# Optimization experiments

Hardware: AMD Instinct MI355X
Metric: run time of the kernel (lower is better)

The kernel has to match this reference:

```python
import jax, jax.numpy as jnp
import numpy as np

B, L, H = 2, 2048, 1024
E = H * 2          # mamba_dim = model_dim * expansion_factor
K = 4              # conv kernel size
N = 16             # SSM state dim
DT_RANK = H // 8   # 128, mamba default ceil(d_model/16) scaled on d_inner


def setup_inputs() -> dict:
    key = jax.random.key(0)
    ks = jax.random.split(key, 12)
    s = lambda fan_in: 1.0 / np.sqrt(fan_in)
    return {
        "x": jax.random.normal(ks[0], (B, L, H), jnp.float32),
        "W_in": jax.random.normal(ks[1], (H, 2 * E), jnp.float32) * s(H),
        "b_in": jnp.zeros((2 * E,), jnp.float32),
        "conv_w": jax.random.normal(ks[2], (E, 1, K), jnp.float32) * s(K),  # depthwise OIH
        "conv_b": jnp.zeros((E,), jnp.float32),
        "x_proj_w": jax.random.normal(ks[3], (E, DT_RANK + 2 * N), jnp.float32) * s(E),
        "dt_proj_w": jax.random.normal(ks[4], (DT_RANK, E), jnp.float32) * s(DT_RANK),
        "dt_bias": jax.random.uniform(ks[5], (E,), jnp.float32, -4.0, -2.0),  # softplus(.) small
        "A_log": jnp.log(jnp.broadcast_to(jnp.arange(1, N + 1, dtype=jnp.float32), (E, N))),
        "D_param": jnp.ones((E,), jnp.float32),
        "W_out": jax.random.normal(ks[6], (E, H), jnp.float32) * s(E),
        "b_out": jnp.zeros((H,), jnp.float32),
    }


def _selective_scan(u, delta, A, Bm, Cm, Dp):
    # u, delta: (B,L,E); A: (E,N); Bm, Cm: (B,L,N); Dp: (E,)
    def step(h, inp):
        d_t, u_t, b_t, c_t = inp          # (B,E), (B,E), (B,N), (B,N)
        dA = jnp.exp(d_t[..., None] * A)  # (B,E,N)
        h = dA * h + (d_t * u_t)[..., None] * b_t[:, None, :]
        y = jnp.einsum("ben,bn->be", h, c_t)
        return h, y

    h0 = jnp.zeros((u.shape[0], A.shape[0], A.shape[1]), u.dtype)
    xs = (delta.transpose(1, 0, 2), u.transpose(1, 0, 2),
          Bm.transpose(1, 0, 2), Cm.transpose(1, 0, 2))
    _, ys = jax.lax.scan(step, h0, xs)    # ys: (L,B,E)
    return ys.transpose(1, 0, 2) + u * Dp


def reference(x, W_in, b_in, conv_w, conv_b, x_proj_w, dt_proj_w, dt_bias,
              A_log, D_param, W_out, b_out):
    silu = jax.nn.silu
    z = x @ W_in + b_in                    # (B,L,2E)
    xc, xr = z[..., :E], z[..., E:]
    xr = silu(xr)
    # causal depthwise conv1d: left-pad K-1 (== torch pad=K-1 then truncate to L)
    xt = xc.transpose(0, 2, 1)             # (B,E,L)
    xt = jax.lax.conv_general_dilated(
        xt, conv_w, window_strides=(1,), padding=[(K - 1, 0)],
        feature_group_count=E, dimension_numbers=("NCH", "OIH", "NCH"))
    xc = silu((xt + conv_b[None, :, None]).transpose(0, 2, 1))  # (B,L,E)
    # S6 selective SSM
    proj = xc @ x_proj_w                   # (B,L,dt_rank+2N)
    dt = proj[..., :DT_RANK]
    Bm = proj[..., DT_RANK:DT_RANK + N]
    Cm = proj[..., DT_RANK + N:]
    delta = jax.nn.softplus(dt @ dt_proj_w + dt_bias)  # (B,L,E)
    A = -jnp.exp(A_log)                    # (E,N)
    y = _selective_scan(xc, delta, A, Bm, Cm, D_param)
    y = y * xr                             # gate
    return y @ W_out + b_out
```

## Files before the change

### kernel.cpp

```cpp
#include <hip/hip_runtime.h>
#include <cstdint>

#define SL 2048
#define SE 2048
#define SB 2
#define SN 16
#define SC 64
#define ST 32

enum { EP_SPLIT_SILU = 1, EP_BIAS = 3, EP_PARTIAL = 4 };

typedef __attribute__((ext_vector_type(8))) short bf16x8;
typedef __attribute__((ext_vector_type(4))) float f32x4;

__device__ __forceinline__ float silu_f(float x) { return x / (1.f + __expf(-x)); }
__device__ __forceinline__ float softplus_f(float x) {
    return (x > 20.f) ? x : log1pf(__expf(x));
}
__device__ __forceinline__ ushort f2bf(float f) {
    union { float f; unsigned u; } a; a.f = f;
    unsigned r = a.u + 0x7fff + ((a.u >> 16) & 1);
    return (ushort)(r >> 16);
}
__device__ __forceinline__ float bf2f(ushort u) {
    union { float f; unsigned u; } a; a.u = ((unsigned)u) << 16;
    return a.f;
}
__device__ __forceinline__ void gload16(const void* g, void* l) {
    __builtin_amdgcn_global_load_lds(
        (const __attribute__((address_space(1))) unsigned int*)g,
        (__attribute__((address_space(3))) unsigned int*)l, 16, 0, 0);
}

template <int MODE>
__global__ __launch_bounds__(512, 1) void hgemm256c(
    const ushort* __restrict__ A, const ushort* __restrict__ Bt,
    float* __restrict__ C, const float* __restrict__ bias,
    float* __restrict__ out2, int M, int N, int K, int Esplit, int KS)
{
    __shared__ ushort As[2][256 * 32];
    __shared__ ushort Bs[2][256 * 32];
    const int tid = threadIdx.x;
    const int w = tid >> 6, l = tid & 63;
    const int wr = w >> 2, wc = w & 3;
    const int m0 = blockIdx.y * 256, n0 = blockIdx.x * 256;
    const int z = blockIdx.z;
    const int kbeg = z * KS;
    const int nt = KS / 32;
    const int srow = l >> 2;
    const int scol = (l & 3) * 8;

    f32x4 acc[8][4];
#pragma unroll
    for (int m = 0; m < 8; m++)
#pragma unroll
        for (int n = 0; n < 4; n++) acc[m][n] = (f32x4)(0.f);

    auto stage = [&](int buf, int t) {
        const int k0 = kbeg + t * 32;
#pragma unroll
        for (int r = 0; r < 2; r++) {
            const int row = w * 32 + r * 16 + srow;
            int brow = n0 + row; if (brow > N - 1) brow = N - 1;
            gload16(A + (size_t)(m0 + row) * K + k0 + scol,
                    &As[buf][(w * 32 + r * 16) * 32]);
            gload16(Bt + (size_t)brow * K + k0 + scol,
                    &Bs[buf][(w * 32 + r * 16) * 32]);
        }
    };

    stage(0, 0);

    int cur = 0;
    const int fr = l & 15, kc = (l >> 4) * 8;
    for (int t = 0; t < nt; t++) {
        if (t + 1 < nt) {
            stage(cur ^ 1, t + 1);
            asm volatile("s_waitcnt vmcnt(4)" ::: "memory");
        } else {
            asm volatile("s_waitcnt vmcnt(0)" ::: "memory");
        }
        __builtin_amdgcn_s_barrier();

        bf16x8 af[8], bfr[4];
#pragma unroll
        for (int m = 0; m < 8; m++)
            af[m] = *(const bf16x8*)&As[cur][(wr * 128 + m * 16 + fr) * 32 + kc];
#pragma unroll
        for (int n = 0; n < 4; n++)
            bfr[n] = *(const bf16x8*)&Bs[cur][(wc * 64 + n * 16 + fr) * 32 + kc];
#pragma unroll
        for (int m = 0; m < 8; m++)
#pragma unroll
            for (int n = 0; n < 4; n++)
                acc[m][n] = __builtin_amdgcn_mfma_f32_16x16x32_bf16(
                    af[m], bfr[n], acc[m][n], 0, 0, 0);

        __builtin_amdgcn_s_barrier();
        cur ^= 1;
    }

    const int cr = (l >> 4) * 4, cc = l & 15;
    float* pbase = C + (size_t)z * M * N;
#pragma unroll
    for (int m = 0; m < 8; m++) {
#pragma unroll
        for (int j = 0; j < 4; j++) {
            const int row = m0 + wr * 128 + m * 16 + cr + j;
#pragma unroll
            for (int n = 0; n < 4; n++) {
                const int col = n0 + wc * 64 + n * 16 + cc;
                float v = acc[m][n][j];
                if (MODE == EP_SPLIT_SILU) {
                    v += bias[col];
                    if (col < Esplit)
                        C[(size_t)row * Esplit + col] = v;
                    else
                        out2[(size_t)row * Esplit + (col - Esplit)] = silu_f(v);
                } else {
                    if (col < N) pbase[(size_t)row * N + col] = v;
                }
            }
        }
    }
}

__global__ __launch_bounds__(512, 1) void g1_gemm(
    const ushort* __restrict__ A, const ushort* __restrict__ Bt,
    float* __restrict__ C, const float* __restrict__ bias,
    float* __restrict__ out2, int M, int N, int K, int Esplit, int KS);

template <int MODE>
__device__ __forceinline__ void gemm_body(
    const ushort* __restrict__ A, const ushort* __restrict__ Bt,
    float* __restrict__ C, const float* __restrict__ bias,
    float* __restrict__ out2, int M, int N, int K, int Esplit, int KS)
{
    __shared__ ushort As[128 * 64];
    __shared__ ushort Bs[128 * 64];
    const int tid = threadIdx.x;
    const int w = tid >> 6, l = tid & 63;
    const int wr = w >> 1, wc = w & 1;
    const int m0 = blockIdx.y * 128, n0 = blockIdx.x * 128;
    const int z = blockIdx.z;
    const int kbeg = z * KS;
    const int nt = KS / 64;
    const int srow = l >> 3, scol = (l & 7) * 8;
    const int fr = l & 15, kc = (l >> 4) * 8;

    f32x4 acc[4][4];
#pragma unroll
    for (int m = 0; m < 4; m++)
#pragma unroll
        for (int n = 0; n < 4; n++) acc[m][n] = (f32x4)(0.f);

    for (int t = 0; t < nt; t++) {
        const int k0 = kbeg + t * 64;
#pragma unroll
        for (int r = 0; r < 4; r++) {
            const int row = r * 32 + w * 8 + srow;
            int brow = n0 + row; if (brow > N - 1) brow = N - 1;
            gload16(A + (size_t)(m0 + row) * K + k0 + scol,
                    &As[r * 2048 + w * 512]);
            gload16(Bt + (size_t)brow * K + k0 + scol,
                    &Bs[r * 2048 + w * 512]);
        }
        __syncthreads();
#pragma unroll
        for (int kk = 0; kk < 64; kk += 32) {
            bf16x8 af[4], bfr[4];
#pragma unroll
            for (int m = 0; m < 4; m++)
                af[m] = *(const bf16x8*)&As[(wr * 64 + m * 16 + fr) * 64 + kk + kc];
#pragma unroll
            for (int n = 0; n < 4; n++)
                bfr[n] = *(const bf16x8*)&Bs[(wc * 64 + n * 16 + fr) * 64 + kk + kc];
#pragma unroll
            for (int m = 0; m < 4; m++)
#pragma unroll
                for (int n = 0; n < 4; n++)
                    acc[m][n] = __builtin_amdgcn_mfma_f32_16x16x32_bf16(
                        af[m], bfr[n], acc[m][n], 0, 0, 0);
        }
        __syncthreads();
    }

    const int cr = (l >> 4) * 4, cc = l & 15;
    float* pbase = C + (size_t)z * M * N;
#pragma unroll
    for (int m = 0; m < 4; m++) {
#pragma unroll
        for (int j = 0; j < 4; j++) {
            const int row = m0 + wr * 64 + m * 16 + cr + j;
#pragma unroll
            for (int n = 0; n < 4; n++) {
                const int col = n0 + wc * 64 + n * 16 + cc;
                float v = acc[m][n][j];
                if (MODE == EP_BIAS) {
                    C[(size_t)row * N + col] = v + bias[col];
                } else {
                    if (col < N) pbase[(size_t)row * N + col] = v;
                }
            }
        }
    }
}

__global__ __launch_bounds__(512, 1) void g1_gemm256(
    const ushort* __restrict__ A, const ushort* __restrict__ Bt,
    float* __restrict__ C, const float* __restrict__ bias,
    float* __restrict__ out2, int M, int N, int K, int Esplit, int KS)
{
}

__global__ __launch_bounds__(256) void g3_gemm(
    const ushort* __restrict__ A, const ushort* __restrict__ Bt,
    float* __restrict__ C, int M, int N, int K, int KS)
{ gemm_body<EP_PARTIAL>(A, Bt, C, nullptr, nullptr, M, N, K, 0, KS); }

__global__ __launch_bounds__(256) void g4_gemm(
    const ushort* __restrict__ A, const ushort* __restrict__ Bt,
    ushort* __restrict__ draw, const float* __restrict__ bias, int M, int N)
{
    __shared__ ushort As[128 * 64];
    __shared__ ushort Bs[128 * 64];
    const int tid = threadIdx.x;
    const int w = tid >> 6, l = tid & 63;
    const int wr = w >> 1, wc = w & 1;
    const int m0 = blockIdx.y * 128, n0 = blockIdx.x * 128;
    const int srow = l >> 3, scol = (l & 7) * 8;
    const int K = 128;

    f32x4 acc[4][4];
#pragma unroll
    for (int m = 0; m < 4; m++)
#pragma unroll
        for (int n = 0; n < 4; n++) acc[m][n] = (f32x4)(0.f);

    const int fr = l & 15, kc = (l >> 4) * 8;
#pragma unroll
    for (int t = 0; t < 2; t++) {
        const int k0 = t * 64;
#pragma unroll
        for (int r = 0; r < 4; r++) {
            const int row = r * 32 + w * 8 + srow;
            gload16(A + (size_t)(m0 + row) * K + k0 + scol, &As[r * 2048 + w * 512]);
            gload16(Bt + (size_t)(n0 + row) * K + k0 + scol, &Bs[r * 2048 + w * 512]);
        }
        __syncthreads();
#pragma unroll
        for (int kk = 0; kk < 64; kk += 32) {
            bf16x8 af[4], bfr[4];
#pragma unroll
            for (int m = 0; m < 4; m++)
                af[m] = *(const bf16x8*)&As[(wr * 64 + m * 16 + fr) * 64 + kk + kc];
#pragma unroll
            for (int n = 0; n < 4; n++)
                bfr[n] = *(const bf16x8*)&Bs[(wc * 64 + n * 16 + fr) * 64 + kk + kc];
#pragma unroll
            for (int m = 0; m < 4; m++)
#pragma unroll
                for (int n = 0; n < 4; n++)
                    acc[m][n] = __builtin_amdgcn_mfma_f32_16x16x32_bf16(
                        af[m], bfr[n], acc[m][n], 0, 0, 0);
        }
        __syncthreads();
    }

    const int cr = (l >> 4) * 4, cc = l & 15;
#pragma unroll
    for (int m = 0; m < 4; m++) {
#pragma unroll
        for (int j = 0; j < 4; j++) {
            const int row = m0 + wr * 64 + m * 16 + cr + j;
#pragma unroll
            for (int n = 0; n < 4; n++) {
                const int col = n0 + wc * 64 + n * 16 + cc;
                draw[(size_t)row * N + col] = f2bf(acc[m][n][j] + bias[col]);
            }
        }
    }
}

__global__ __launch_bounds__(256) void gemm3_reduce(
    const float* __restrict__ Pp, float* __restrict__ proj,
    ushort* __restrict__ dtbf, int M, int N, int Z)
{
    const size_t g = (size_t)blockIdx.x * 256 + threadIdx.x;
    const size_t tot = (size_t)M * N;
    if (g >= tot) return;
    float s = 0.f;
    for (int z = 0; z < Z; z++) s += Pp[(size_t)z * tot + g];
    proj[g] = s;
    const int col = (int)(g % N);
    if (col < 128) {
        const size_t row = g / N;
        dtbf[row * 128 + col] = f2bf(s);
    }
}

__global__ __launch_bounds__(256) void reduce6(
    const float* __restrict__ Pp, const float* __restrict__ bias,
    float* __restrict__ out, int M, int N, int Z)
{
    const size_t g = (size_t)blockIdx.x * 256 + threadIdx.x;
    const size_t tot4 = (size_t)M * N / 4;
    if (g >= tot4) return;
    const int n4 = N / 4;
    float4 s = ((const float4*)bias)[g % n4];
    for (int z = 0; z < Z; z++) {
        float4 p = ((const float4*)Pp)[z * tot4 + g];
        s.x += p.x; s.y += p.y; s.z += p.z; s.w += p.w;
    }
    ((float4*)out)[g] = s;
}

__global__ __launch_bounds__(256) void f2bf_vec(
    const float* __restrict__ in, ushort* __restrict__ out, size_t n4)
{
    for (size_t i = (size_t)blockIdx.x * 256 + threadIdx.x; i < n4;
         i += (size_t)gridDim.x * 256) {
        float4 v = ((const float4*)in)[i];
        ushort4 o;
        o.x = f2bf(v.x); o.y = f2bf(v.y); o.z = f2bf(v.z); o.w = f2bf(v.w);
        ((ushort4*)out)[i] = o;
    }
}

__global__ __launch_bounds__(256) void f2bf_transpose(
    const float* __restrict__ W, ushort* __restrict__ Wt, int R, int Ccols)
{
    __shared__ float tile[32][33];
    const int bc = blockIdx.x * 32, br = blockIdx.y * 32;
    const int tx = threadIdx.x & 31, ty = threadIdx.x >> 5;
    for (int i = ty; i < 32; i += 8)
        tile[i][tx] = W[(size_t)(br + i) * Ccols + bc + tx];
    __syncthreads();
    for (int i = ty; i < 32; i += 8)
        Wt[(size_t)(bc + i) * R + br + tx] = f2bf(tile[tx][i]);
}

__global__ __launch_bounds__(256) void conv_silu4(
    const float* __restrict__ xin, const float* __restrict__ w,
    const float* __restrict__ cb, ushort* __restrict__ xobf,
    int Ln, int En, size_t total4)
{
    const int Eq = En >> 2;
    for (size_t idx = (size_t)blockIdx.x * 256 + threadIdx.x; idx < total4;
         idx += (size_t)gridDim.x * 256) {
        const int e4 = (int)(idx % Eq);
        const size_t row = idx / Eq;
        const int l = (int)(row % Ln);
        float4 acc = ((const float4*)cb)[e4];
        const float4 w0 = ((const float4*)w)[e4 * 4 + 0];
        const float4 w1 = ((const float4*)w)[e4 * 4 + 1];
        const float4 w2 = ((const float4*)w)[e4 * 4 + 2];
        const float4 w3 = ((const float4*)w)[e4 * 4 + 3];
        const float wt0[4] = {w0.x, w0.y, w0.z, w0.w};
        const float wt1[4] = {w1.x, w1.y, w1.z, w1.w};
        const float wt2[4] = {w2.x, w2.y, w2.z, w2.w};
        const float wt3[4] = {w3.x, w3.y, w3.z, w3.w};
#pragma unroll
        for (int k = 0; k < 4; k++) {
            if (l - 3 + k >= 0) {
                float4 xv = ((const float4*)xin)[(row - 3 + k) * Eq + e4];
                acc.x = fmaf(wt0[k], xv.x, acc.x);
                acc.y = fmaf(wt1[k], xv.y, acc.y);
                acc.z = fmaf(wt2[k], xv.z, acc.z);
                acc.w = fmaf(wt3[k], xv.w, acc.w);
            }
        }
        ushort4 o;
        o.x = f2bf(silu_f(acc.x)); o.y = f2bf(silu_f(acc.y));
        o.z = f2bf(silu_f(acc.z)); o.w = f2bf(silu_f(acc.w));
        ((ushort4*)xobf)[idx] = o;
    }
}

__global__ __launch_bounds__(256) void scan_pass1(
    const ushort* __restrict__ draw, const ushort* __restrict__ u,
    const float* __restrict__ proj, const float* __restrict__ A_log,
    float* __restrict__ Pbuf, float* __restrict__ Sbuf)
{
    __shared__ float sB[ST * SN];
    const int tid = threadIdx.x;
    const int eb = blockIdx.x & 7;
    const int c  = (blockIdx.x >> 3) & (SC - 1);
    const int b  = blockIdx.x >> 9;
    const int e  = eb * 256 + tid;
    const size_t row0 = (size_t)b * SL + c * ST;

    for (int i = tid; i < ST * SN; i += 256) {
        const int tl = i >> 4, n = i & 15;
        sB[i] = proj[(row0 + tl) * 160 + 128 + n];
    }
    __syncthreads();

    float An[SN], h[SN];
    {
        const float4* Ap = (const float4*)(A_log + (size_t)e * SN);
#pragma unroll
        for (int q = 0; q < 4; q++) {
            float4 v = Ap[q];
            An[q * 4 + 0] = -expf(v.x);
            An[q * 4 + 1] = -expf(v.y);
            An[q * 4 + 2] = -expf(v.z);
            An[q * 4 + 3] = -expf(v.w);
        }
    }
#pragma unroll
    for (int n = 0; n < SN; n++) h[n] = 0.f;

    float dsum = 0.f;
    size_t idx = row0 * SE + e;
    float d = softplus_f(bf2f(draw[idx])), uu = bf2f(u[idx]);
    for (int tl = 0; tl < ST; tl++) {
        ushort dn = 0, un = 0;
        if (tl + 1 < ST) { dn = draw[idx + SE]; un = u[idx + SE]; }
        const float du = d * uu;
        dsum += d;
#pragma unroll
        for (int n = 0; n < SN; n++) {
            const float dA = __expf(d * An[n]);
            h[n] = fmaf(dA, h[n], du * sB[tl * SN + n]);
        }
        d = softplus_f(bf2f(dn)); uu = bf2f(un); idx += SE;
    }

    const size_t ob = ((((size_t)c * SB) + b) * SE + e) * SN;
#pragma unroll
    for (int q = 0; q < 4; q++) {
        float4 pv, sv;
        pv.x = __expf(An[q * 4 + 0] * dsum); sv.x = h[q * 4 + 0];
        pv.y = __expf(An[q * 4 + 1] * dsum); sv.y = h[q * 4 + 1];
        pv.z = __expf(An[q * 4 + 2] * dsum); sv.z = h[q * 4 + 2];
        pv.w = __expf(An[q * 4 + 3] * dsum); sv.w = h[q * 4 + 3];
        *(float4*)(Pbuf + ob + q * 4) = pv;
        *(float4*)(Sbuf + ob + q * 4) = sv;
    }
}

__global__ __launch_bounds__(256) void scan_pass2(
    const float* __restrict__ Pbuf, const float* __restrict__ Sbuf,
    float* __restrict__ hinit)
{
    const size_t g = (size_t)blockIdx.x * 256 + threadIdx.x;
    const size_t stride = (size_t)SB * SE * SN;
    float h = 0.f;
    float P = Pbuf[g], S = Sbuf[g];
    for (int c = 0; c < SC; c++) {
        float Pn = 0.f, Sn = 0.f;
        if (c + 1 < SC) {
            Pn = Pbuf[(c + 1) * stride + g];
            Sn = Sbuf[(c + 1) * stride + g];
        }
        hinit[c * stride + g] = h;
        h = fmaf(P, h, S);
        P = Pn; S = Sn;
    }
}

__global__ __launch_bounds__(256) void scan_pass3(
    const ushort* __restrict__ draw, const ushort* __restrict__ u,
    const float* __restrict__ proj, const float* __restrict__ A_log,
    const float* __restrict__ Dp, const float* __restrict__ xr,
    const float* __restrict__ hinit, ushort* __restrict__ yg)
{
    __shared__ float sB[ST * SN];
    __shared__ float sC[ST * SN];
    const int tid = threadIdx.x;
    const int eb = blockIdx.x & 7;
    const int c  = (blockIdx.x >> 3) & (SC - 1);
    const int b  = blockIdx.x >> 9;
    const int e  = eb * 256 + tid;
    const size_t row0 = (size_t)b * SL + c * ST;

    for (int i = tid; i < ST * SN; i += 256) {
        const int tl = i >> 4, n = i & 15;
        sB[i] = proj[(row0 + tl) * 160 + 128 + n];
        sC[i] = proj[(row0 + tl) * 160 + 144 + n];
    }
    __syncthreads();

    float An[SN], h[SN];
    {
        const float4* Ap = (const float4*)(A_log + (size_t)e * SN);
#pragma unroll
        for (int q = 0; q < 4; q++) {
            float4 v = Ap[q];
            An[q * 4 + 0] = -expf(v.x);
            An[q * 4 + 1] = -expf(v.y);
            An[q * 4 + 2] = -expf(v.z);
            An[q * 4 + 3] = -expf(v.w);
        }
    }
    {
        const size_t ib = ((((size_t)c * SB) + b) * SE + e) * SN;
#pragma unroll
        for (int q = 0; q < 4; q++) {
            float4 v = *(const float4*)(hinit + ib + q * 4);
            h[q * 4 + 0] = v.x; h[q * 4 + 1] = v.y;
            h[q * 4 + 2] = v.z; h[q * 4 + 3] = v.w;
        }
    }
    const float De = Dp[e];

    size_t idx = row0 * SE + e;
    float d = softplus_f(bf2f(draw[idx])), uu = bf2f(u[idx]), g = xr[idx];
    for (int tl = 0; tl < ST; tl++) {
        ushort dn = 0, un = 0;
        float gn = 0.f;
        if (tl + 1 < ST) {
            dn = draw[idx + SE]; un = u[idx + SE]; gn = xr[idx + SE];
        }
        const float du = d * uu;
        float y = 0.f;
#pragma unroll
        for (int n = 0; n < SN; n++) {
            const float dA = __expf(d * An[n]);
            h[n] = fmaf(dA, h[n], du * sB[tl * SN + n]);
            y = fmaf(h[n], sC[tl * SN + n], y);
        }
        yg[idx] = f2bf((y + uu * De) * g);
        d = softplus_f(bf2f(dn)); uu = bf2f(un); g = gn; idx += SE;
    }
}

extern "C" void kernel_launch(void* const* d_in, const int* in_sizes, int n_in,
                              void* d_out, int out_size, void* d_ws, size_t ws_size,
                              hipStream_t stream)
{
    const int Bc = 2, Lc = 2048, Hc = 1024, Ec = 2048;
    const int M = Bc * Lc;
    const int PN = 160;
    const int SKZ = 8;
    const int SK6 = 4;

    const float* x        = (const float*)d_in[0];
    const float* W_in     = (const float*)d_in[1];
    const float* b_in     = (const float*)d_in[2];
    const float* conv_w   = (const float*)d_in[3];
    const float* conv_b   = (const float*)d_in[4];
    const float* x_proj_w = (const float*)d_in[5];
    const float* dt_proj_w= (const float*)d_in[6];
    const float* dt_bias  = (const float*)d_in[7];
    const float* A_log    = (const float*)d_in[8];
    const float* D_param  = (const float*)d_in[9];
    const float* W_out    = (const float*)d_in[10];
    const float* b_out    = (const float*)d_in[11];
    float* out = (float*)d_out;

    float* ws = (float*)d_ws;
    const size_t ME = (size_t)M * Ec;
    const size_t PS = (size_t)SB * SE * SC * SN;

    float* xc_raw = ws;
    float* xr     = xc_raw + ME;
    float* r2     = xr + ME;
    float* r3     = r2 + ME;
    float* proj   = r3 + ME;
    float* hinit  = proj + (size_t)M * PN;

    ushort* xbf    = (ushort*)r3;
    ushort* W_in_t = (ushort*)r2;
    ushort* xc_bf  = (ushort*)r2;
    ushort* draw   = (ushort*)r3;
    float*  Pp3    = xc_raw;
    ushort* xpw_t  = (ushort*)hinit;
    ushort* dtw_t  = (ushort*)hinit + 327680;
    ushort* dtbf   = (ushort*)hinit + 327680 + 262144;
    float*  Pbuf   = xc_raw;
    float*  Sbuf   = xc_raw + PS;
    ushort* ygbf   = (ushort*)xc_raw;
    ushort* W_out_t= (ushort*)r3;
    float*  Pp6    = xr;

    f2bf_vec<<<1024, 256, 0, stream>>>(x, xbf, (size_t)M * Hc / 4);
    f2bf_transpose<<<dim3(2 * Ec / 32, Hc / 32), 256, 0, stream>>>(
        W_in, W_in_t, Hc, 2 * Ec);
    f2bf_transpose<<<dim3(PN / 32, Ec / 32), 256, 0, stream>>>(
        x_proj_w, xpw_t, Ec, PN);
    f2bf_transpose<<<dim3(Ec / 32, 128 / 32), 256, 0, stream>>>(
        dt_proj_w, dtw_t, 128, Ec);

    hgemm256c<EP_SPLIT_SILU><<<dim3(2 * Ec / 256, M / 256, 1), 512, 0, stream>>>(
        xbf, W_in_t, xc_raw, b_in, xr, M, 2 * Ec, Hc, Ec, Hc);

    conv_silu4<<<2048, 256, 0, stream>>>(
        xc_raw, conv_w, conv_b, xc_bf, Lc, Ec, ME / 4);

    g3_gemm<<<dim3(2, M / 128, SKZ), 256, 0, stream>>>(
        xc_bf, xpw_t, Pp3, M, PN, Ec, Ec / SKZ);
    gemm3_reduce<<<(M * PN + 255) / 256, 256, 0, stream>>>(
        Pp3, proj, dtbf, M, PN, SKZ);

    g4_gemm<<<dim3(Ec / 128, M / 128), 256, 0, stream>>>(
        dtbf, dtw_t, draw, dt_bias, M, Ec);

    scan_pass1<<<SB * SC * (SE / 256), 256, 0, stream>>>(
        draw, xc_bf, proj, A_log, Pbuf, Sbuf);
    scan_pass2<<<(SB * SE * SN) / 256, 256, 0, stream>>>(Pbuf, Sbuf, hinit);
    scan_pass3<<<SB * SC * (SE / 256), 256, 0, stream>>>(
        draw, xc_bf, proj, A_log, D_param, xr, hinit, ygbf);

    f2bf_transpose<<<dim3(Hc / 32, Ec / 32), 256, 0, stream>>>(
        W_out, W_out_t, Ec, Hc);

    hgemm256c<EP_PARTIAL><<<dim3(Hc / 256, M / 256, SK6), 512, 0, stream>>>(
        ygbf, W_out_t, Pp6, nullptr, nullptr, M, Hc, Ec, 0, Ec / SK6);
    reduce6<<<(int)((size_t)M * Hc / 4 + 255) / 256, 256, 0, stream>>>(
        Pp6, b_out, out, M, Hc, SK6);
}
```

Measured before the change: 310.8 us.

## Restructure 256x256 GEMM with BK=64, XOR-swizzled LDS, and interleaved quadrant pipeline

The 256-tile bf16 GEMM used by the input and output projections now stages K=64 per iteration instead of 32 and applies an XOR swizzle to LDS rows to avoid bank conflicts. Each iteration is split into four quadrant phases whose global prefetches of A and B are spread across phases, with s_setprio raised around the MFMA bursts. The aim is fewer barriers per K, better overlap of loads with math and conflict-free LDS reads. In exchange LDS use doubles to 128 KB and the N-bound clamp on B rows is dropped, which assumes N is a multiple of 256.

```diff
diff --git a/kernel.cpp b/kernel.cpp
--- a/kernel.cpp
+++ b/kernel.cpp
@@ -33,22 +33,23 @@
 }
 
 template <int MODE>
-__global__ __launch_bounds__(512, 1) void hgemm256c(
+__global__ __launch_bounds__(512, 1) void hgemm8p(
     const ushort* __restrict__ A, const ushort* __restrict__ Bt,
     float* __restrict__ C, const float* __restrict__ bias,
     float* __restrict__ out2, int M, int N, int K, int Esplit, int KS)
 {
-    __shared__ ushort As[2][256 * 32];
-    __shared__ ushort Bs[2][256 * 32];
+    __shared__ ushort As[2][256 * 64];
+    __shared__ ushort Bs[2][256 * 64];
     const int tid = threadIdx.x;
     const int w = tid >> 6, l = tid & 63;
     const int wr = w >> 2, wc = w & 3;
     const int m0 = blockIdx.y * 256, n0 = blockIdx.x * 256;
     const int z = blockIdx.z;
     const int kbeg = z * KS;
-    const int nt = KS / 32;
-    const int srow = l >> 2;
-    const int scol = (l & 3) * 8;
+    const int nt = KS / 64;
+
+    const int srow_w = w * 8 + (l >> 3);
+    const int skel   = 8 * ((l & 7) ^ (l >> 3));
 
     f32x4 acc[8][4];
 #pragma unroll
@@ -56,48 +57,121 @@
 #pragma unroll
         for (int n = 0; n < 4; n++) acc[m][n] = (f32x4)(0.f);
 
-    auto stage = [&](int buf, int t) {
-        const int k0 = kbeg + t * 32;
-#pragma unroll
-        for (int r = 0; r < 2; r++) {
-            const int row = w * 32 + r * 16 + srow;
-            int brow = n0 + row; if (brow > N - 1) brow = N - 1;
-            gload16(A + (size_t)(m0 + row) * K + k0 + scol,
-                    &As[buf][(w * 32 + r * 16) * 32]);
-            gload16(Bt + (size_t)brow * K + k0 + scol,
-                    &Bs[buf][(w * 32 + r * 16) * 32]);
+    auto stageA = [&](int slot, int t) {
+        const int k0 = kbeg + t * 64;
+#pragma unroll
+        for (int q = 0; q < 4; q++) {
+            const int row = q * 64 + srow_w;
+            gload16(A + (size_t)(m0 + row) * K + k0 + skel,
+                    &As[slot][q * 4096 + w * 512]);
         }
     };
-
-    stage(0, 0);
-
-    int cur = 0;
-    const int fr = l & 15, kc = (l >> 4) * 8;
+    auto stageB = [&](int slot, int t) {
+        const int k0 = kbeg + t * 64;
+#pragma unroll
+        for (int q = 0; q < 4; q++) {
+            const int row = q * 64 + srow_w;
+            gload16(Bt + (size_t)(n0 + row) * K + k0 + skel,
+                    &Bs[slot][q * 4096 + w * 512]);
+        }
+    };
+
+    const int fr  = l & 15;
+    const int kxo = ((l >> 4) * 16);
+    const int swz = (l & 7) << 4;
+    auto aoff = [&](int m, int ks) {
+        const int row = wr * 128 + m * 16 + fr;
+        return row * 64 + (((ks * 64 + kxo) ^ swz) >> 1);
+    };
+    auto boff = [&](int n, int ks) {
+        const int row = wc * 64 + n * 16 + fr;
+        return row * 64 + (((ks * 64 + kxo) ^ swz) >> 1);
+    };
+
+    stageA(0, 0);
+    stageB(0, 0);
+    asm volatile("s_waitcnt vmcnt(0)" ::: "memory");
+    __syncthreads();
+
     for (int t = 0; t < nt; t++) {
-        if (t + 1 < nt) {
-            stage(cur ^ 1, t + 1);
-            asm volatile("s_waitcnt vmcnt(4)" ::: "memory");
-        } else {
-            asm volatile("s_waitcnt vmcnt(0)" ::: "memory");
-        }
+        const int s = t & 1;
+        const bool pf = (t + 1 < nt);
+        bf16x8 af[4][2], bf[2][2], bf2[2][2];
+
+        if (pf) stageA(s ^ 1, t + 1);
+#pragma unroll
+        for (int m = 0; m < 4; m++)
+#pragma unroll
+            for (int ks = 0; ks < 2; ks++)
+                af[m][ks] = *(const bf16x8*)&As[s][aoff(m, ks)];
+#pragma unroll
+        for (int n = 0; n < 2; n++)
+#pragma unroll
+            for (int ks = 0; ks < 2; ks++)
+                bf[n][ks] = *(const bf16x8*)&Bs[s][boff(n, ks)];
+        __builtin_amdgcn_s_setprio(1);
+#pragma unroll
+        for (int m = 0; m < 4; m++)
+#pragma unroll
+            for (int n = 0; n < 2; n++)
+#pragma unroll
+                for (int ks = 0; ks < 2; ks++)
+                    acc[m][n] = __builtin_amdgcn_mfma_f32_16x16x32_bf16(
+                        af[m][ks], bf[n][ks], acc[m][n], 0, 0, 0);
+        __builtin_amdgcn_s_setprio(0);
         __builtin_amdgcn_s_barrier();
 
-        bf16x8 af[8], bfr[4];
-#pragma unroll
-        for (int m = 0; m < 8; m++)
-            af[m] = *(const bf16x8*)&As[cur][(wr * 128 + m * 16 + fr) * 32 + kc];
-#pragma unroll
-        for (int n = 0; n < 4; n++)
-            bfr[n] = *(const bf16x8*)&Bs[cur][(wc * 64 + n * 16 + fr) * 32 + kc];
-#pragma unroll
-        for (int m = 0; m < 8; m++)
-#pragma unroll
-            for (int n = 0; n < 4; n++)
-                acc[m][n] = __builtin_amdgcn_mfma_f32_16x16x32_bf16(
-                    af[m], bfr[n], acc[m][n], 0, 0, 0);
-
+        if (pf) stageB(s ^ 1, t + 1);
+#pragma unroll
+        for (int n = 0; n < 2; n++)
+#pragma unroll
+            for (int ks = 0; ks < 2; ks++)
+                bf2[n][ks] = *(const bf16x8*)&Bs[s][boff(2 + n, ks)];
+        __builtin_amdgcn_s_setprio(1);
+#pragma unroll
+        for (int m = 0; m < 4; m++)
+#pragma unroll
+            for (int n = 0; n < 2; n++)
+#pragma unroll
+                for (int ks = 0; ks < 2; ks++)
+                    acc[m][2 + n] = __builtin_amdgcn_mfma_f32_16x16x32_bf16(
+                        af[m][ks], bf2[n][ks], acc[m][2 + n], 0, 0, 0);
+        __builtin_amdgcn_s_setprio(0);
         __builtin_amdgcn_s_barrier();
-        cur ^= 1;
+
+#pragma unroll
+        for (int m = 0; m < 4; m++)
+#pragma unroll
+            for (int ks = 0; ks < 2; ks++)
+                af[m][ks] = *(const bf16x8*)&As[s][aoff(4 + m, ks)];
+        __builtin_amdgcn_s_setprio(1);
+#pragma unroll
+        for (int m = 0; m < 4; m++)
+#pragma unroll
+            for (int n = 0; n < 2; n++)
+#pragma unroll
+                for (int ks = 0; ks < 2; ks++)
+                    acc[4 + m][2 + n] = __builtin_amdgcn_mfma_f32_16x16x32_bf16(
+                        af[m][ks], bf2[n][ks], acc[4 + m][2 + n], 0, 0, 0);
+        __builtin_amdgcn_s_setprio(0);
+        __builtin_amdgcn_s_barrier();
+
+#pragma unroll
+        for (int n = 0; n < 2; n++)
+#pragma unroll
+            for (int ks = 0; ks < 2; ks++)
+                bf[n][ks] = *(const bf16x8*)&Bs[s][boff(n, ks)];
+        __builtin_amdgcn_s_setprio(1);
+#pragma unroll
+        for (int m = 0; m < 4; m++)
+#pragma unroll
+            for (int n = 0; n < 2; n++)
+#pragma unroll
+                for (int ks = 0; ks < 2; ks++)
+                    acc[4 + m][n] = __builtin_amdgcn_mfma_f32_16x16x32_bf16(
+                        af[m][ks], bf[n][ks], acc[4 + m][n], 0, 0, 0);
+        __builtin_amdgcn_s_setprio(0);
+        __syncthreads();
     }
 
     const int cr = (l >> 4) * 4, cc = l & 15;
@@ -125,11 +199,6 @@
     }
 }
 
-__global__ __launch_bounds__(512, 1) void g1_gemm(
-    const ushort* __restrict__ A, const ushort* __restrict__ Bt,
-    float* __restrict__ C, const float* __restrict__ bias,
-    float* __restrict__ out2, int M, int N, int K, int Esplit, int KS);
-
 template <int MODE>
 __device__ __forceinline__ void gemm_body(
     const ushort* __restrict__ A, const ushort* __restrict__ Bt,
@@ -204,13 +273,6 @@
             }
         }
     }
-}
-
-__global__ __launch_bounds__(512, 1) void g1_gemm256(
-    const ushort* __restrict__ A, const ushort* __restrict__ Bt,
-    float* __restrict__ C, const float* __restrict__ bias,
-    float* __restrict__ out2, int M, int N, int K, int Esplit, int KS)
-{
 }
 
 __global__ __launch_bounds__(256) void g3_gemm(
@@ -583,7 +645,7 @@
     f2bf_transpose<<<dim3(Ec / 32, 128 / 32), 256, 0, stream>>>(
         dt_proj_w, dtw_t, 128, Ec);
 
-    hgemm256c<EP_SPLIT_SILU><<<dim3(2 * Ec / 256, M / 256, 1), 512, 0, stream>>>(
+    hgemm8p<EP_SPLIT_SILU><<<dim3(2 * Ec / 256, M / 256, 1), 512, 0, stream>>>(
         xbf, W_in_t, xc_raw, b_in, xr, M, 2 * Ec, Hc, Ec, Hc);
 
     conv_silu4<<<2048, 256, 0, stream>>>(
@@ -606,7 +668,7 @@
     f2bf_transpose<<<dim3(Hc / 32, Ec / 32), 256, 0, stream>>>(
         W_out, W_out_t, Ec, Hc);
 
-    hgemm256c<EP_PARTIAL><<<dim3(Hc / 256, M / 256, SK6), 512, 0, stream>>>(
+    hgemm8p<EP_PARTIAL><<<dim3(Hc / 256, M / 256, SK6), 512, 0, stream>>>(
         ygbf, W_out_t, Pp6, nullptr, nullptr, M, Hc, Ec, 0, Ec / SK6);
     reduce6<<<(int)((size_t)M * Hc / 4 + 255) / 256, 256, 0, stream>>>(
         Pp6, b_out, out, M, Hc, SK6);
```

After: 309.0 us. Within noise of the previous version (-0.6%).
